# Performance work log

Measured on AMD Instinct MI355X. Metric: run time of the kernel, lower is better.

The kernel has to match this reference:

```python
import jax, jax.numpy as jnp
import numpy as np

HEADS = 8
DIM_HEAD = 64
BOTTLENECK = 40


def setup_inputs() -> dict:
    key = jax.random.key(0)
    ks = jax.random.split(key, 10)
    b, n, qs = 4, 1024, 256
    inner = HEADS * DIM_HEAD
    s = lambda fan_in: 1.0 / np.sqrt(fan_in)
    return {
        "x":   jax.random.normal(ks[0], (b, n, qs), dtype=jnp.float32),
        # weights stored as (in, out) so forward is x @ W
        "wq1": jax.random.normal(ks[1], (qs, BOTTLENECK), dtype=jnp.float32) * s(qs),
        "wq2": jax.random.normal(ks[2], (BOTTLENECK, inner), dtype=jnp.float32) * s(BOTTLENECK),
        "wk1": jax.random.normal(ks[3], (qs, BOTTLENECK), dtype=jnp.float32) * s(qs),
        "wk2": jax.random.normal(ks[4], (BOTTLENECK, inner), dtype=jnp.float32) * s(BOTTLENECK),
        "wv1": jax.random.normal(ks[5], (qs, BOTTLENECK), dtype=jnp.float32) * s(qs),
        "wv2": jax.random.normal(ks[6], (BOTTLENECK, inner), dtype=jnp.float32) * s(BOTTLENECK),
        "wo":  jax.random.normal(ks[7], (inner, qs), dtype=jnp.float32) * s(inner),
        "bo":  jax.random.normal(ks[8], (qs,), dtype=jnp.float32) * 0.01,
    }


def reference(x, wq1, wq2, wk1, wk2, wv1, wv2, wo, bo):
    b, n, _ = x.shape
    h, d = HEADS, DIM_HEAD
    scale = d ** -0.5

    # bottlenecked QKV projections (40-dim), SiLU on K bottleneck
    q = (x @ wq1) @ wq2                       # (b, n, h*d)
    k = jax.nn.silu(x @ wk1) @ wk2            # (b, n, h*d)
    v = (x @ wv1) @ wv2                       # (b, n, h*d)

    def split(t):  # 'b n (h d) -> b (h n) d'
        return t.reshape(b, n, h, d).transpose(0, 2, 1, 3).reshape(b, h * n, d)

    q, k, v = split(q), split(k), split(v)

    sim = jnp.einsum('bid,bjd->bij', q, k) * scale   # (b, h*n, h*n)
    attn = jax.nn.softmax(sim, axis=-1)
    out = jnp.einsum('bij,bjd->bid', attn, v)        # (b, h*n, d)

    # 'b (h n) d -> b n (h d)'
    out = out.reshape(b, h, n, d).transpose(0, 2, 1, 3).reshape(b, n, h * d)
    return out @ wo + bo
```

## Files before the change

### kernel.cpp

```cpp
#include <hip/hip_runtime.h>
#include <hip/hip_bf16.h>


#define B_    4
#define H_    8
#define NSEQ  1024
#define SEQ   8192
#define DH    64
#define QS    256
#define INNER 512
#define QSCALE 0.18033688011112042f

#define KVSW_BATCH 524288
#define OPHALF (2097152)

typedef __bf16 bf16x8 __attribute__((ext_vector_type(8)));
typedef float floatx4 __attribute__((ext_vector_type(4)));

__global__ __launch_bounds__(256) void conv_kernel(
    const float* __restrict__ wq1, const float* __restrict__ wk1,
    const float* __restrict__ wv1,
    const float* __restrict__ wq2, const float* __restrict__ wk2,
    const float* __restrict__ wv2,
    const float* __restrict__ wo,
    __hip_bfloat16* __restrict__ W1BH, __hip_bfloat16* __restrict__ W1BL,
    __hip_bfloat16* __restrict__ W2BH, __hip_bfloat16* __restrict__ W2BL,
    __hip_bfloat16* __restrict__ WOBH, __hip_bfloat16* __restrict__ WOBL)
{
  const int tid = threadIdx.x;
  const int blk = blockIdx.x;

  if (blk < 16) {
    const int t  = blk * 256 + tid;
    const int n  = t & 127;
    const int kq = t >> 7;
    const int kc = kq >> 2, q = kq & 3;
    const float* src; int col;
    if (n < 40)       { src = wq1; col = n; }
    else if (n < 80)  { src = wk1; col = n - 40; }
    else if (n < 120) { src = wv1; col = n - 80; }
    else              { src = nullptr; col = 0; }
    bf16x8 hv, lv;
    #pragma unroll
    for (int j = 0; j < 8; ++j) {
      const int k = kc * 32 + q * 8 + j;
      const float v = src ? src[k * 40 + col] : 0.f;
      const __bf16 h16 = (__bf16)v;
      hv[j] = h16; lv[j] = (__bf16)(v - (float)h16);
    }
    const size_t off = (((size_t)(n >> 4) * 8 + kc) * 64 + (n & 15) + 16 * q) * 8;
    *(bf16x8*)(W1BH + off) = hv;
    *(bf16x8*)(W1BL + off) = lv;
  } else if (blk < 64) {
    const int t  = (blk - 16) * 256 + tid;
    const int n  = t & 511;
    const int r  = t >> 9;
    const int p  = r >> 3;
    const int kq = r & 7;
    const int kc = kq >> 2, q = kq & 3;
    const float* w2 = (p == 0) ? wq2 : (p == 1) ? wk2 : wv2;
    bf16x8 hv, lv;
    #pragma unroll
    for (int j = 0; j < 8; ++j) {
      const int k = kc * 32 + q * 8 + j;
      const float v = (k < 40) ? w2[(size_t)k * 512 + n] : 0.f;
      const __bf16 h16 = (__bf16)v;
      hv[j] = h16; lv[j] = (__bf16)(v - (float)h16);
    }
    const size_t off = ((((size_t)p * 32 + (n >> 4)) * 2 + kc) * 64 + (n & 15) + 16 * q) * 8;
    *(bf16x8*)(W2BH + off) = hv;
    *(bf16x8*)(W2BL + off) = lv;
  } else {
    const int cid = blk - 64;
    const int t4  = (cid * 256 + tid) * 4;
    const int n   = t4 & 255;
    const int k8  = t4 >> 8;
    float4 rr[8];
    #pragma unroll
    for (int kk = 0; kk < 8; ++kk)
      rr[kk] = *(const float4*)(wo + (size_t)(k8 * 8 + kk) * QS + n);
    const int kc = k8 >> 2, qq = k8 & 3;
    #pragma unroll
    for (int nn = 0; nn < 4; ++nn) {
      const int nc = n + nn;
      const int l  = (nc & 15) + 16 * qq;
      const size_t off = ((size_t)((nc >> 4) * 16 + kc) * 64 + l) * 8;
      bf16x8 hv, lv;
      #pragma unroll
      for (int kk = 0; kk < 8; ++kk) {
        const float v = (nn == 0) ? rr[kk].x : (nn == 1) ? rr[kk].y
                      : (nn == 2) ? rr[kk].z : rr[kk].w;
        const __bf16 h16 = (__bf16)v;
        hv[kk] = h16;
        lv[kk] = (__bf16)(v - (float)h16);
      }
      *(bf16x8*)(WOBH + off) = hv;
      *(bf16x8*)(WOBL + off) = lv;
    }
  }
}

__global__ __launch_bounds__(512) void qkv_kernel(
    const float* __restrict__ x,
    const __hip_bfloat16* __restrict__ W1BH, const __hip_bfloat16* __restrict__ W1BL,
    const __hip_bfloat16* __restrict__ W2BH, const __hip_bfloat16* __restrict__ W2BL,
    __hip_bfloat16* __restrict__ Qg, __hip_bfloat16* __restrict__ KSg,
    __hip_bfloat16* __restrict__ VSg)
{
  const int tid  = threadIdx.x;
  const int b    = blockIdx.x >> 6;
  const int nblk = blockIdx.x & 63;
  const int n0   = nblk << 4;
  const int wave = tid >> 6;
  const int lane = tid & 63;
  const int m    = lane & 15;
  const int q    = lane >> 4;

  __shared__ __align__(16) float xs[16][260];
  __shared__ __align__(16) float tb32[16][140];
  __shared__ __align__(16) __hip_bfloat16 qb[8320];
  __shared__ __align__(16) __hip_bfloat16 kb[8320];
  __shared__ __align__(16) __hip_bfloat16 vb[10240];

  #pragma unroll
  for (int j = 0; j < 2; ++j) {
    const int i  = tid + j * 512;
    const int r  = i >> 6;
    const int c4 = (i & 63) << 2;
    *(float4*)(&xs[r][c4]) =
        *(const float4*)(x + ((size_t)b * NSEQ + n0 + r) * QS + c4);
  }
  __syncthreads();

  bf16x8 xh[8], xl[8];
  #pragma unroll
  for (int kc = 0; kc < 8; ++kc) {
    const float4 f0 = *(const float4*)(&xs[m][kc * 32 + q * 8]);
    const float4 f1 = *(const float4*)(&xs[m][kc * 32 + q * 8 + 4]);
    float v[8] = {f0.x, f0.y, f0.z, f0.w, f1.x, f1.y, f1.z, f1.w};
    #pragma unroll
    for (int j = 0; j < 8; ++j) {
      const __bf16 h16 = (__bf16)v[j];
      xh[kc][j] = h16;
      xl[kc][j] = (__bf16)(v[j] - (float)h16);
    }
  }

  {
    floatx4 hh = (floatx4){0.f, 0.f, 0.f, 0.f};
    floatx4 hl = (floatx4){0.f, 0.f, 0.f, 0.f};
    floatx4 lh = (floatx4){0.f, 0.f, 0.f, 0.f};
    const __hip_bfloat16* w1h = W1BH + ((size_t)wave * 8 * 64 + lane) * 8;
    const __hip_bfloat16* w1l = W1BL + ((size_t)wave * 8 * 64 + lane) * 8;
    #pragma unroll
    for (int kc = 0; kc < 8; ++kc) {
      const bf16x8 bh = *(const bf16x8*)(w1h + kc * 512);
      const bf16x8 bl = *(const bf16x8*)(w1l + kc * 512);
      hh = __builtin_amdgcn_mfma_f32_16x16x32_bf16(xh[kc], bh, hh, 0, 0, 0);
      hl = __builtin_amdgcn_mfma_f32_16x16x32_bf16(xh[kc], bl, hl, 0, 0, 0);
      lh = __builtin_amdgcn_mfma_f32_16x16x32_bf16(xl[kc], bh, lh, 0, 0, 0);
    }
    const int n1 = wave * 16 + m;
    #pragma unroll
    for (int r = 0; r < 4; ++r) {
      float d = (hh[r] + hl[r]) + lh[r];
      if (n1 >= 40 && n1 < 80) d = d / (1.f + __expf(-d));
      tb32[q * 4 + r][n1] = d;
    }
  }
  __syncthreads();

  #pragma unroll
  for (int p = 0; p < 3; ++p) {
    bf16x8 a2h[2], a2l[2];
    {
      const float4 g0 = *(const float4*)(&tb32[m][p * 40 + q * 8]);
      const float4 g1 = *(const float4*)(&tb32[m][p * 40 + q * 8 + 4]);
      float v[8] = {g0.x, g0.y, g0.z, g0.w, g1.x, g1.y, g1.z, g1.w};
      #pragma unroll
      for (int j = 0; j < 8; ++j) {
        const __bf16 h16 = (__bf16)v[j];
        a2h[0][j] = h16;
        a2l[0][j] = (__bf16)(v[j] - (float)h16);
      }
    }
    if (q == 0) {
      const float4 g0 = *(const float4*)(&tb32[m][p * 40 + 32]);
      const float4 g1 = *(const float4*)(&tb32[m][p * 40 + 36]);
      float v[8] = {g0.x, g0.y, g0.z, g0.w, g1.x, g1.y, g1.z, g1.w};
      #pragma unroll
      for (int j = 0; j < 8; ++j) {
        const __bf16 h16 = (__bf16)v[j];
        a2h[1][j] = h16;
        a2l[1][j] = (__bf16)(v[j] - (float)h16);
      }
    } else {
      #pragma unroll
      for (int j = 0; j < 8; ++j) { a2h[1][j] = (__bf16)0.f; a2l[1][j] = (__bf16)0.f; }
    }

    #pragma unroll
    for (int i = 0; i < 4; ++i) {
      const int nt = wave * 4 + i;
      floatx4 sHH = (floatx4){0.f, 0.f, 0.f, 0.f};
      floatx4 sHL = (floatx4){0.f, 0.f, 0.f, 0.f};
      floatx4 sLH = (floatx4){0.f, 0.f, 0.f, 0.f};
      #pragma unroll
      for (int kc = 0; kc < 2; ++kc) {
        const size_t boff = (((size_t)(p * 32 + nt) * 2 + kc) * 64 + lane) * 8;
        const bf16x8 bh = *(const bf16x8*)(W2BH + boff);
        const bf16x8 bl = *(const bf16x8*)(W2BL + boff);
        sHH = __builtin_amdgcn_mfma_f32_16x16x32_bf16(a2h[kc], bh, sHH, 0, 0, 0);
        sHL = __builtin_amdgcn_mfma_f32_16x16x32_bf16(a2h[kc], bl, sHL, 0, 0, 0);
        sLH = __builtin_amdgcn_mfma_f32_16x16x32_bf16(a2l[kc], bh, sLH, 0, 0, 0);
      }
      const int nn = nt * 16 + m;
      #pragma unroll
      for (int r = 0; r < 4; ++r) {
        const int row = q * 4 + r;
        const float d = (sHH[r] + sHL[r]) + sLH[r];
        if (p == 0)      qb[row * 520 + nn] = __float2bfloat16(d * QSCALE);
        else if (p == 1) kb[row * 520 + nn] = __float2bfloat16(d);
        else             vb[nn * 20 + row]  = __float2bfloat16(d);
      }
    }
  }
  __syncthreads();

  #pragma unroll
  for (int j = 0; j < 2; ++j) {
    const int i  = tid + j * 512;
    const int h  = i >> 7;
    const int r  = (i >> 3) & 15;
    const int d8 = i & 7;
    *(float4*)(Qg + ((size_t)b * SEQ + h * NSEQ + n0 + r) * DH + d8 * 8) =
        *(const float4*)(&qb[r * 520 + h * 64 + d8 * 8]);
  }
  #pragma unroll
  for (int j = 0; j < 2; ++j) {
    const int i    = tid + j * 512;
    const int h    = i >> 7;
    const int ks2  = (i >> 6) & 1;
    const int quad = (i >> 4) & 3;
    const int r    = i & 15;
    const int ln   = quad * 16 + r;
    const size_t dst = (size_t)b * KVSW_BATCH
        + ((size_t)((h * 64 + nblk) * 2 + ks2) * 64 + ln) * 8;
    *(float4*)(KSg + dst) = *(const float4*)(&kb[r * 520 + h * 64 + ks2 * 32 + quad * 8]);
  }
  {
    const int st  = nblk & 1;
    const int p32 = nblk >> 1;
    #pragma unroll
    for (int pass = 0; pass < 4; ++pass) {
      const int i   = tid + pass * 512;
      const int h   = i >> 8;
      const int dnt = (i >> 6) & 3;
      const int dm  = (i >> 2) & 15;
      const int rg  = i & 3;
      const int ln  = rg * 16 + dm;
      const size_t dst = (size_t)b * KVSW_BATCH
          + ((size_t)((h * 32 + p32) * 4 + dnt) * 64 + ln) * 8 + st * 4;
      *(uint2*)(VSg + dst) = *(const uint2*)(&vb[(h * 64 + dnt * 16 + dm) * 20 + rg * 4]);
    }
  }
}

struct PairBuf {
  bf16x8 k[2][2];
  bf16x8 v[4];
};

__global__ __launch_bounds__(256, 3) void attn_kernel(
    const __hip_bfloat16* __restrict__ Qg,
    const __hip_bfloat16* __restrict__ KSg,
    const __hip_bfloat16* __restrict__ VSg,
    float* __restrict__ OPg,
    float* __restrict__ PSg)
{
  __shared__ float Osh[4][16][68];
  __shared__ float psums[4][64];

  const int tid  = threadIdx.x;
  const int wave = tid >> 6;
  const int lane = tid & 63;
  const int lrow = lane & 15;
  const int quad = lane >> 4;

  const int xcd   = blockIdx.x & 7;
  const int idx   = blockIdx.x >> 3;
  const int b     = xcd >> 1;
  const int half  = idx & 1;
  const int qtile = (xcd & 1) * 64 + (idx >> 1);
  const int qbase = qtile * 64;

  const __hip_bfloat16* Qb  = Qg + ((size_t)b * SEQ + qbase) * DH;
  const __hip_bfloat16* kp0 = KSg + (size_t)b * KVSW_BATCH + half * 262144
                              + (size_t)wave * 65536 + lane * 8;
  const __hip_bfloat16* vp0 = VSg + (size_t)b * KVSW_BATCH + half * 262144
                              + (size_t)wave * 65536 + lane * 8;

  bf16x8 qf[4][2];
  #pragma unroll
  for (int mt = 0; mt < 4; ++mt)
    #pragma unroll
    for (int s = 0; s < 2; ++s)
      qf[mt][s] = *(const bf16x8*)(Qb + (mt * 16 + lrow) * DH + s * 32 + quad * 8);

  floatx4 oacc[4][4];
  #pragma unroll
  for (int mt = 0; mt < 4; ++mt)
    #pragma unroll
    for (int dnt = 0; dnt < 4; ++dnt)
      oacc[mt][dnt] = (floatx4){0.f, 0.f, 0.f, 0.f};
  float psum[4] = {0.f, 0.f, 0.f, 0.f};

  #pragma unroll 2
  for (int pair = 0; pair < 32; ++pair) {
    PairBuf pb;
    const __hip_bfloat16* kp = kp0 + pair * 2048;
    pb.k[0][0] = *(const bf16x8*)(kp);
    pb.k[0][1] = *(const bf16x8*)(kp + 512);
    pb.k[1][0] = *(const bf16x8*)(kp + 1024);
    pb.k[1][1] = *(const bf16x8*)(kp + 1536);
    const __hip_bfloat16* vp = vp0 + pair * 2048;
    #pragma unroll
    for (int dnt = 0; dnt < 4; ++dnt)
      pb.v[dnt] = *(const bf16x8*)(vp + dnt * 512);

    #pragma unroll
    for (int mt = 0; mt < 4; ++mt) {
      floatx4 s0 = (floatx4){0.f, 0.f, 0.f, 0.f};
      floatx4 s1 = (floatx4){0.f, 0.f, 0.f, 0.f};
      s0 = __builtin_amdgcn_mfma_f32_16x16x32_bf16(pb.k[0][0], qf[mt][0], s0, 0, 0, 0);
      s0 = __builtin_amdgcn_mfma_f32_16x16x32_bf16(pb.k[0][1], qf[mt][1], s0, 0, 0, 0);
      s1 = __builtin_amdgcn_mfma_f32_16x16x32_bf16(pb.k[1][0], qf[mt][0], s1, 0, 0, 0);
      s1 = __builtin_amdgcn_mfma_f32_16x16x32_bf16(pb.k[1][1], qf[mt][1], s1, 0, 0, 0);
      float p[8];
      #pragma unroll
      for (int r = 0; r < 4; ++r) {
        p[r]     = __builtin_amdgcn_exp2f(s0[r]);
        p[4 + r] = __builtin_amdgcn_exp2f(s1[r]);
      }
      psum[mt] += ((p[0] + p[1]) + (p[2] + p[3])) + ((p[4] + p[5]) + (p[6] + p[7]));
      bf16x8 pa;
      #pragma unroll
      for (int j = 0; j < 8; ++j) pa[j] = (__bf16)p[j];
      #pragma unroll
      for (int dnt = 0; dnt < 4; ++dnt)
        oacc[mt][dnt] = __builtin_amdgcn_mfma_f32_16x16x32_bf16(pa, pb.v[dnt], oacc[mt][dnt], 0, 0, 0);
    }
  }

  #pragma unroll
  for (int mt = 0; mt < 4; ++mt) {
    float s = psum[mt];
    s += __shfl_xor(s, 16, 64);
    s += __shfl_xor(s, 32, 64);
    psum[mt] = s;
  }
  if (quad == 0) {
    #pragma unroll
    for (int mt = 0; mt < 4; ++mt)
      psums[wave][mt * 16 + lrow] = psum[mt];
  }

  const size_t opbase = ((size_t)half * B_ + b) * SEQ + qbase;

  #pragma unroll
  for (int mt = 0; mt < 4; ++mt) {
    #pragma unroll
    for (int dnt = 0; dnt < 4; ++dnt)
      #pragma unroll
      for (int r = 0; r < 4; ++r)
        Osh[wave][quad * 4 + r][dnt * 16 + lrow] = oacc[mt][dnt][r];
    __syncthreads();

    {
      const int q16 = tid >> 4;
      const int d0  = (tid & 15) * 4;
      float4 a0 = *(const float4*)(&Osh[0][q16][d0]);
      float4 a1 = *(const float4*)(&Osh[1][q16][d0]);
      float4 a2 = *(const float4*)(&Osh[2][q16][d0]);
      float4 a3 = *(const float4*)(&Osh[3][q16][d0]);
      float4 res;
      res.x = (a0.x + a1.x) + (a2.x + a3.x);
      res.y = (a0.y + a1.y) + (a2.y + a3.y);
      res.z = (a0.z + a1.z) + (a2.z + a3.z);
      res.w = (a0.w + a1.w) + (a2.w + a3.w);
      *(float4*)(OPg + (opbase + mt * 16 + q16) * DH + d0) = res;
    }
    if (mt == 0 && tid < 64) {
      const float tot = (psums[0][tid] + psums[1][tid]) + (psums[2][tid] + psums[3][tid]);
      PSg[opbase + tid] = tot;
    }
    __syncthreads();
  }
}

__global__ __launch_bounds__(256, 1) void out_kernel(
    const float* __restrict__ OPg, const float* __restrict__ PSg,
    const __hip_bfloat16* __restrict__ WOBH, const __hip_bfloat16* __restrict__ WOBL,
    const float* __restrict__ bo, float* __restrict__ out)
{
  __shared__ __align__(16) __hip_bfloat16 apH[8192];
  __shared__ __align__(16) __hip_bfloat16 apL[8192];
  __shared__ float invs[16][8];

  const int tid  = threadIdx.x;
  const int b    = blockIdx.x >> 6;
  const int n0   = (blockIdx.x & 63) << 4;
  const int lane = tid & 63;
  const int wave = tid >> 6;

  if (tid < 128) {
    const int r = tid >> 3, h = tid & 7;
    const size_t row = (size_t)b * SEQ + h * NSEQ + n0 + r;
    invs[r][h] = 1.0f / (PSg[row] + PSg[(size_t)B_ * SEQ + row]);
  }
  __syncthreads();

  {
    const int m   = tid & 15;
    const int q   = (tid >> 4) & 3;
    const int kc0 = tid >> 6;
    #pragma unroll
    for (int pss = 0; pss < 4; ++pss) {
      const int kc = kc0 + pss * 4;
      const int h  = kc >> 1;
      const int dh = (q + 4 * (kc & 1)) * 8;
      const size_t idx = (((size_t)b * H_ + h) * NSEQ + n0 + m) * DH + dh;
      const float4 a0 = *(const float4*)(OPg + idx);
      const float4 a1 = *(const float4*)(OPg + idx + 4);
      const float4 b0 = *(const float4*)(OPg + OPHALF + idx);
      const float4 b1 = *(const float4*)(OPg + OPHALF + idx + 4);
      const float inv = invs[m][h];
      float v[8];
      v[0] = (a0.x + b0.x) * inv; v[1] = (a0.y + b0.y) * inv;
      v[2] = (a0.z + b0.z) * inv; v[3] = (a0.w + b0.w) * inv;
      v[4] = (a1.x + b1.x) * inv; v[5] = (a1.y + b1.y) * inv;
      v[6] = (a1.z + b1.z) * inv; v[7] = (a1.w + b1.w) * inv;
      bf16x8 hv, lv;
      #pragma unroll
      for (int j = 0; j < 8; ++j) {
        const __bf16 h16 = (__bf16)v[j];
        hv[j] = h16;
        lv[j] = (__bf16)(v[j] - (float)h16);
      }
      const int off = (kc * 64 + (m + 16 * q)) * 8;
      *(bf16x8*)(apH + off) = hv;
      *(bf16x8*)(apL + off) = lv;
    }
  }
  __syncthreads();

  bf16x8 ah[16], al[16];
  #pragma unroll
  for (int kc = 0; kc < 16; ++kc) {
    ah[kc] = *(const bf16x8*)(apH + (kc * 64 + lane) * 8);
    al[kc] = *(const bf16x8*)(apL + (kc * 64 + lane) * 8);
  }

  const int colq = lane & 15;
  const int quad = lane >> 4;

  #pragma unroll
  for (int nt4 = 0; nt4 < 4; ++nt4) {
    const int nt = nt4 * 4 + wave;
    const __hip_bfloat16* wbh = WOBH + ((size_t)nt * 16 * 64 + lane) * 8;
    const __hip_bfloat16* wbl = WOBL + ((size_t)nt * 16 * 64 + lane) * 8;
    floatx4 aHH = (floatx4){0.f, 0.f, 0.f, 0.f};
    floatx4 aHL = (floatx4){0.f, 0.f, 0.f, 0.f};
    floatx4 aLH = (floatx4){0.f, 0.f, 0.f, 0.f};
    #pragma unroll
    for (int kg = 0; kg < 4; ++kg) {
      bf16x8 bh[4], bl[4];
      #pragma unroll
      for (int j = 0; j < 4; ++j) {
        bh[j] = *(const bf16x8*)(wbh + (kg * 4 + j) * 512);
        bl[j] = *(const bf16x8*)(wbl + (kg * 4 + j) * 512);
      }
      #pragma unroll
      for (int j = 0; j < 4; ++j) {
        const int kc = kg * 4 + j;
        aHH = __builtin_amdgcn_mfma_f32_16x16x32_bf16(ah[kc], bh[j], aHH, 0, 0, 0);
        aHL = __builtin_amdgcn_mfma_f32_16x16x32_bf16(ah[kc], bl[j], aHL, 0, 0, 0);
        aLH = __builtin_amdgcn_mfma_f32_16x16x32_bf16(al[kc], bh[j], aLH, 0, 0, 0);
      }
    }
    const int n  = nt * 16 + colq;
    const float bv = bo[n];
    #pragma unroll
    for (int r = 0; r < 4; ++r) {
      const int mm = quad * 4 + r;
      out[((size_t)b * NSEQ + n0 + mm) * QS + n] =
          ((aHH[r] + aHL[r]) + aLH[r]) + bv;
    }
  }
}

extern "C" void kernel_launch(void* const* d_in, const int* in_sizes, int n_in,
                              void* d_out, int out_size, void* d_ws, size_t ws_size,
                              hipStream_t stream) {
  const float* x   = (const float*)d_in[0];
  const float* wq1 = (const float*)d_in[1];
  const float* wq2 = (const float*)d_in[2];
  const float* wk1 = (const float*)d_in[3];
  const float* wk2 = (const float*)d_in[4];
  const float* wv1 = (const float*)d_in[5];
  const float* wv2 = (const float*)d_in[6];
  const float* wo  = (const float*)d_in[7];
  const float* bo  = (const float*)d_in[8];
  float* out = (float*)d_out;

  __hip_bfloat16* Qg  = (__hip_bfloat16*)d_ws;
  __hip_bfloat16* KSg = Qg + (size_t)B_ * SEQ * DH;
  __hip_bfloat16* VSg = KSg + (size_t)B_ * KVSW_BATCH;
  float*          OPg = (float*)(VSg + (size_t)B_ * KVSW_BATCH);
  float*          PSg = OPg + 2 * (size_t)B_ * SEQ * DH;
  __hip_bfloat16* WOBH = (__hip_bfloat16*)(PSg + 2 * (size_t)B_ * SEQ);
  __hip_bfloat16* WOBL = WOBH + (size_t)INNER * QS;
  __hip_bfloat16* W1BH = WOBL + (size_t)INNER * QS;
  __hip_bfloat16* W1BL = W1BH + 32768;
  __hip_bfloat16* W2BH = W1BL + 32768;
  __hip_bfloat16* W2BL = W2BH + 98304;

  conv_kernel<<<80, 256, 0, stream>>>(wq1, wk1, wv1, wq2, wk2, wv2, wo,
                                      W1BH, W1BL, W2BH, W2BL, WOBH, WOBL);
  qkv_kernel<<<256, 512, 0, stream>>>(x, W1BH, W1BL, W2BH, W2BL, Qg, KSg, VSg);
  attn_kernel<<<1024, 256, 0, stream>>>(Qg, KSg, VSg, OPg, PSg);
  out_kernel<<<256, 256, 0, stream>>>(OPg, PSg, WOBH, WOBL, bo, out);
}
```

Baseline: 166.0 us.

## Merge KV halves into one 512-thread attention block, drop partial-output combine

The attention kernel now runs 8 waves per block covering the full key range, instead of two 256-thread blocks each covering half the keys. The partial outputs are reduced in shared memory across 8 waves, so the global two-half partial buffer and its summation in the output kernel go away. This removes the extra global writes and reads of the second partial output and row sums. In exchange the grid is halved, occupancy bounds change to 512x2, and the 8-way shared-memory reduction is done by only half the threads.

```diff
diff --git a/kernel.cpp b/kernel.cpp
--- a/kernel.cpp
+++ b/kernel.cpp
@@ -12,7 +12,6 @@
 #define QSCALE 0.18033688011112042f
 
 #define KVSW_BATCH 524288
-#define OPHALF (2097152)
 
 typedef __bf16 bf16x8 __attribute__((ext_vector_type(8)));
 typedef float floatx4 __attribute__((ext_vector_type(4)));
@@ -271,15 +270,15 @@
   bf16x8 v[4];
 };
 
-__global__ __launch_bounds__(256, 3) void attn_kernel(
+__global__ __launch_bounds__(512, 2) void attn_kernel(
     const __hip_bfloat16* __restrict__ Qg,
     const __hip_bfloat16* __restrict__ KSg,
     const __hip_bfloat16* __restrict__ VSg,
     float* __restrict__ OPg,
     float* __restrict__ PSg)
 {
-  __shared__ float Osh[4][16][68];
-  __shared__ float psums[4][64];
+  __shared__ float Osh[8][16][68];
+  __shared__ float psums[8][64];
 
   const int tid  = threadIdx.x;
   const int wave = tid >> 6;
@@ -290,14 +289,13 @@
   const int xcd   = blockIdx.x & 7;
   const int idx   = blockIdx.x >> 3;
   const int b     = xcd >> 1;
-  const int half  = idx & 1;
-  const int qtile = (xcd & 1) * 64 + (idx >> 1);
+  const int qtile = (xcd & 1) * 64 + idx;
   const int qbase = qtile * 64;
 
   const __hip_bfloat16* Qb  = Qg + ((size_t)b * SEQ + qbase) * DH;
-  const __hip_bfloat16* kp0 = KSg + (size_t)b * KVSW_BATCH + half * 262144
+  const __hip_bfloat16* kp0 = KSg + (size_t)b * KVSW_BATCH
                               + (size_t)wave * 65536 + lane * 8;
-  const __hip_bfloat16* vp0 = VSg + (size_t)b * KVSW_BATCH + half * 262144
+  const __hip_bfloat16* vp0 = VSg + (size_t)b * KVSW_BATCH
                               + (size_t)wave * 65536 + lane * 8;
 
   bf16x8 qf[4][2];
@@ -365,7 +363,7 @@
       psums[wave][mt * 16 + lrow] = psum[mt];
   }
 
-  const size_t opbase = ((size_t)half * B_ + b) * SEQ + qbase;
+  const size_t opbase = (size_t)b * SEQ + qbase;
 
   #pragma unroll
   for (int mt = 0; mt < 4; ++mt) {
@@ -376,22 +374,27 @@
         Osh[wave][quad * 4 + r][dnt * 16 + lrow] = oacc[mt][dnt][r];
     __syncthreads();
 
-    {
+    if (tid < 256) {
       const int q16 = tid >> 4;
       const int d0  = (tid & 15) * 4;
       float4 a0 = *(const float4*)(&Osh[0][q16][d0]);
       float4 a1 = *(const float4*)(&Osh[1][q16][d0]);
       float4 a2 = *(const float4*)(&Osh[2][q16][d0]);
       float4 a3 = *(const float4*)(&Osh[3][q16][d0]);
+      float4 a4 = *(const float4*)(&Osh[4][q16][d0]);
+      float4 a5 = *(const float4*)(&Osh[5][q16][d0]);
+      float4 a6 = *(const float4*)(&Osh[6][q16][d0]);
+      float4 a7 = *(const float4*)(&Osh[7][q16][d0]);
       float4 res;
-      res.x = (a0.x + a1.x) + (a2.x + a3.x);
-      res.y = (a0.y + a1.y) + (a2.y + a3.y);
-      res.z = (a0.z + a1.z) + (a2.z + a3.z);
-      res.w = (a0.w + a1.w) + (a2.w + a3.w);
+      res.x = ((a0.x + a1.x) + (a2.x + a3.x)) + ((a4.x + a5.x) + (a6.x + a7.x));
+      res.y = ((a0.y + a1.y) + (a2.y + a3.y)) + ((a4.y + a5.y) + (a6.y + a7.y));
+      res.z = ((a0.z + a1.z) + (a2.z + a3.z)) + ((a4.z + a5.z) + (a6.z + a7.z));
+      res.w = ((a0.w + a1.w) + (a2.w + a3.w)) + ((a4.w + a5.w) + (a6.w + a7.w));
       *(float4*)(OPg + (opbase + mt * 16 + q16) * DH + d0) = res;
     }
     if (mt == 0 && tid < 64) {
-      const float tot = (psums[0][tid] + psums[1][tid]) + (psums[2][tid] + psums[3][tid]);
+      const float tot = ((psums[0][tid] + psums[1][tid]) + (psums[2][tid] + psums[3][tid]))
+                      + ((psums[4][tid] + psums[5][tid]) + (psums[6][tid] + psums[7][tid]));
       PSg[opbase + tid] = tot;
     }
     __syncthreads();
@@ -416,7 +419,7 @@
   if (tid < 128) {
     const int r = tid >> 3, h = tid & 7;
     const size_t row = (size_t)b * SEQ + h * NSEQ + n0 + r;
-    invs[r][h] = 1.0f / (PSg[row] + PSg[(size_t)B_ * SEQ + row]);
+    invs[r][h] = 1.0f / PSg[row];
   }
   __syncthreads();
 
@@ -432,14 +435,12 @@
       const size_t idx = (((size_t)b * H_ + h) * NSEQ + n0 + m) * DH + dh;
       const float4 a0 = *(const float4*)(OPg + idx);
       const float4 a1 = *(const float4*)(OPg + idx + 4);
-      const float4 b0 = *(const float4*)(OPg + OPHALF + idx);
-      const float4 b1 = *(const float4*)(OPg + OPHALF + idx + 4);
       const float inv = invs[m][h];
       float v[8];
-      v[0] = (a0.x + b0.x) * inv; v[1] = (a0.y + b0.y) * inv;
-      v[2] = (a0.z + b0.z) * inv; v[3] = (a0.w + b0.w) * inv;
-      v[4] = (a1.x + b1.x) * inv; v[5] = (a1.y + b1.y) * inv;
-      v[6] = (a1.z + b1.z) * inv; v[7] = (a1.w + b1.w) * inv;
+      v[0] = a0.x * inv; v[1] = a0.y * inv;
+      v[2] = a0.z * inv; v[3] = a0.w * inv;
+      v[4] = a1.x * inv; v[5] = a1.y * inv;
+      v[6] = a1.z * inv; v[7] = a1.w * inv;
       bf16x8 hv, lv;
       #pragma unroll
       for (int j = 0; j < 8; ++j) {
@@ -517,8 +518,8 @@
   __hip_bfloat16* KSg = Qg + (size_t)B_ * SEQ * DH;
   __hip_bfloat16* VSg = KSg + (size_t)B_ * KVSW_BATCH;
   float*          OPg = (float*)(VSg + (size_t)B_ * KVSW_BATCH);
-  float*          PSg = OPg + 2 * (size_t)B_ * SEQ * DH;
-  __hip_bfloat16* WOBH = (__hip_bfloat16*)(PSg + 2 * (size_t)B_ * SEQ);
+  float*          PSg = OPg + (size_t)B_ * SEQ * DH;
+  __hip_bfloat16* WOBH = (__hip_bfloat16*)(PSg + (size_t)B_ * SEQ);
   __hip_bfloat16* WOBL = WOBH + (size_t)INNER * QS;
   __hip_bfloat16* W1BH = WOBL + (size_t)INNER * QS;
   __hip_bfloat16* W1BL = W1BH + 32768;
@@ -528,6 +529,6 @@
   conv_kernel<<<80, 256, 0, stream>>>(wq1, wk1, wv1, wq2, wk2, wv2, wo,
                                       W1BH, W1BL, W2BH, W2BL, WOBH, WOBL);
   qkv_kernel<<<256, 512, 0, stream>>>(x, W1BH, W1BL, W2BH, W2BL, Qg, KSg, VSg);
-  attn_kernel<<<1024, 256, 0, stream>>>(Qg, KSg, VSg, OPg, PSg);
+  attn_kernel<<<512, 512, 0, stream>>>(Qg, KSg, VSg, OPg, PSg);
   out_kernel<<<256, 256, 0, stream>>>(OPg, PSg, WOBH, WOBL, bo, out);
 }
```

New measurement: 170.5 us. 2.8% more time.
